# Optimization experiments

Measured on AMD Instinct MI355X. Metric: run time of the kernel, lower is better.

## Reference

```python
import jax, jax.numpy as jnp
import numpy as np

N_NODES = 20000
N_EDGES = 160000
N_GRAPHS = 1000
IN_DIM = 11
HID = 128
EDGE_DIM = 3
N_LAYERS = 5
BN_EPS = 1e-5


def setup_inputs() -> dict:
    key = jax.random.key(0)
    ks = jax.random.split(key, 24)
    x = jax.random.normal(ks[0], (N_NODES, IN_DIM), dtype=jnp.float32)
    edge_index = jax.random.randint(ks[1], (2, N_EDGES), 0, N_NODES, dtype=jnp.int64)
    batch = jnp.sort(jax.random.randint(ks[2], (N_NODES,), 0, N_GRAPHS, dtype=jnp.int64))
    edge_attr = jax.random.uniform(ks[3], (N_EDGES, EDGE_DIM), dtype=jnp.float32)
    s_in = 1.0 / np.sqrt(IN_DIM)
    s_z = 1.0 / np.sqrt(2 * HID + EDGE_DIM)
    s_h = 1.0 / np.sqrt(HID)
    W_in = jax.random.uniform(ks[4], (IN_DIM, HID), minval=-s_in, maxval=s_in)
    b_in = jax.random.uniform(ks[5], (HID,), minval=-s_in, maxval=s_in)
    Wf = jax.random.uniform(ks[6], (N_LAYERS, 2 * HID + EDGE_DIM, HID), minval=-s_z, maxval=s_z)
    bf = jax.random.uniform(ks[7], (N_LAYERS, HID), minval=-s_z, maxval=s_z)
    Ws = jax.random.uniform(ks[8], (N_LAYERS, 2 * HID + EDGE_DIM, HID), minval=-s_z, maxval=s_z)
    bs = jax.random.uniform(ks[9], (N_LAYERS, HID), minval=-s_z, maxval=s_z)
    gamma = jnp.ones((N_LAYERS, HID), dtype=jnp.float32)
    beta = jnp.zeros((N_LAYERS, HID), dtype=jnp.float32)
    W1 = jax.random.uniform(ks[10], (HID, HID), minval=-s_h, maxval=s_h)
    b1 = jax.random.uniform(ks[11], (HID,), minval=-s_h, maxval=s_h)
    W2 = jax.random.uniform(ks[12], (HID, HID), minval=-s_h, maxval=s_h)
    b2 = jax.random.uniform(ks[13], (HID,), minval=-s_h, maxval=s_h)
    W3 = jax.random.uniform(ks[14], (HID, 1), minval=-s_h, maxval=s_h)
    b3 = jax.random.uniform(ks[15], (1,), minval=-s_h, maxval=s_h)
    return {"x": x, "edge_index": edge_index, "batch": batch, "edge_attr": edge_attr,
            "W_in": W_in, "b_in": b_in, "Wf": Wf, "bf": bf, "Ws": Ws, "bs": bs,
            "gamma": gamma, "beta": beta, "W1": W1, "b1": b1, "W2": W2, "b2": b2,
            "W3": W3, "b3": b3}


def reference(x, edge_index, batch, edge_attr, W_in, b_in, Wf, bf, Ws, bs,
              gamma, beta, W1, b1, W2, b2, W3, b3):
    src = edge_index[0]  # x_j (source / neighbor)
    dst = edge_index[1]  # x_i (target / aggregation index)
    # in-degree per node for mean aggregation (zero-degree -> divide by 1, yields 0)
    deg = jax.ops.segment_sum(jnp.ones((N_EDGES,), jnp.float32), dst, num_segments=N_NODES)
    deg = jnp.maximum(deg, 1.0)[:, None]

    h = x @ W_in + b_in  # [N, H]
    for l in range(N_LAYERS):
        # CGConv: z = [x_i, x_j, e]; msg = sigmoid(z Wf) * softplus(z Ws); residual + mean-aggr
        z = jnp.concatenate([h[dst], h[src], edge_attr], axis=-1)  # [E, 2H+D]
        msg = jax.nn.sigmoid(z @ Wf[l] + bf[l]) * jax.nn.softplus(z @ Ws[l] + bs[l])
        agg = jax.ops.segment_sum(msg, dst, num_segments=N_NODES) / deg
        h = h + agg
        # BatchNorm1d (training-mode batch stats, biased variance)
        mu = jnp.mean(h, axis=0)
        var = jnp.mean((h - mu) ** 2, axis=0)
        h = (h - mu) * jax.lax.rsqrt(var + BN_EPS) * gamma[l] + beta[l]
        h = jax.nn.relu(h)
        # dropout omitted (eval mode)

    # global mean pool over graphs
    cnt = jax.ops.segment_sum(jnp.ones((N_NODES,), jnp.float32), batch, num_segments=N_GRAPHS)
    g = jax.ops.segment_sum(h, batch, num_segments=N_GRAPHS) / jnp.maximum(cnt, 1.0)[:, None]

    g = jax.nn.relu(g @ W1 + b1)
    g = jax.nn.relu(g @ W2 + b2)
    return g @ W3 + b3  # [G, 1]
```

## Files before the change

### kernel.cpp

```cpp
#include <hip/hip_runtime.h>
#include <hip/hip_cooperative_groups.h>
#include <math.h>

namespace cg = cooperative_groups;

#define NN 20000
#define NE 160000
#define NG 1000
#define IND 11
#define H 128
#define ED 3
#define NL 5
#define ZDH (259*128)
#define BN_EPSF 1e-5f
#define EPW 32
#define QR 16
#define GP 4
#define MBLK 313
#define NWIN (NE / EPW)
#define MEGA_BLOCKS 1024

#define DEG_BLKS ((NE + 255) / 256)
#define WPREP_BLKS ((NL * 512 * H + 255) / 256)
#define GB_BLKS ((NN + 255) / 256)
#define HIN_BLKS 512
#define PREP_GRID (DEG_BLKS + WPREP_BLKS + GB_BLKS + HIN_BLKS)

typedef unsigned short ushort_t;
typedef unsigned int uint_t;
typedef __attribute__((ext_vector_type(8))) short bf8_t;
typedef __attribute__((ext_vector_type(4))) float f4_t;

__device__ inline ushort_t f2bf(float x) {
    unsigned int u = __float_as_uint(x);
    unsigned int r = (u + 0x7fffu + ((u >> 16) & 1u)) >> 16;
    return (ushort_t)r;
}
__device__ inline float bf2f(ushort_t b) {
    return __uint_as_float(((unsigned int)b) << 16);
}

__global__ __launch_bounds__(256) void prep_fused(const int* __restrict__ dst,
                                                  int* __restrict__ degi,
                                                  const float* __restrict__ Wf,
                                                  const float* __restrict__ Ws,
                                                  ushort_t* __restrict__ Wt,
                                                  const float* __restrict__ x,
                                                  const float* __restrict__ Win,
                                                  const float* __restrict__ bin,
                                                  float* __restrict__ h,
                                                  const int* __restrict__ batch,
                                                  int* __restrict__ gstart) {
    int b = blockIdx.x;
    int tid = threadIdx.x;
    if (b < DEG_BLKS) {
        int e = b * 256 + tid;
        if (e < NE) atomicAdd(&degi[dst[e]], 1);
    } else if (b < DEG_BLKS + WPREP_BLKS) {
        int idx = (b - DEG_BLKS) * 256 + tid;
        if (idx < NL * 512 * H) {
            int k = idx & 127;
            int n = (idx >> 7) & 511;
            int l = idx >> 16;
            int t = n >> 7, j = n & 127;
            const float* W = (t == 0 || t == 2) ? Wf : Ws;
            int krow = (t < 2) ? k : (H + k);
            ushort_t val = f2bf(W[(size_t)l * ZDH + krow * H + j]);
            int nt = j >> 4, sub = j & 15;
            int ks = k >> 5, quad = (k >> 3) & 3, e2 = k & 7;
            int lane = quad * 16 + sub;
            Wt[(size_t)l * 65536 + (size_t)t * 16384 +
               (((nt * 4 + ks) * 64 + lane) * 8 + e2)] = val;
        }
    } else if (b < DEG_BLKS + WPREP_BLKS + GB_BLKS) {
        int n = (b - DEG_BLKS - WPREP_BLKS) * 256 + tid;
        if (n < NN) {
            int b0 = batch[n];
            int bn = (n + 1 < NN) ? batch[n + 1] : NG;
            if (n == 0)
                for (int t = 0; t <= b0; ++t) gstart[t] = 0;
            for (int t = b0 + 1; t <= bn; ++t) gstart[t] = n + 1;
        }
    } else {
        __shared__ float lw[IND * H];
        for (int i = tid; i < IND * H; i += 256) lw[i] = Win[i];
        __syncthreads();
        int j = tid & 127;
        float bj = bin[j];
        int rb = b - (DEG_BLKS + WPREP_BLKS + GB_BLKS);
        for (int n = rb * 2 + (tid >> 7); n < NN; n += HIN_BLKS * 2) {
            const float* xr = x + (size_t)n * IND;
            float acc = bj;
#pragma unroll
            for (int k = 0; k < IND; ++k) acc = fmaf(xr[k], lw[k * H + j], acc);
            h[(size_t)n * H + j] = acc;
        }
    }
}

__global__ __launch_bounds__(256) void reserve_kernel(const int* __restrict__ degi,
                                                      int* __restrict__ cursor,
                                                      float* __restrict__ invdeg,
                                                      int* __restrict__ counter,
                                                      unsigned* __restrict__ endmask) {
    int n = blockIdx.x * blockDim.x + threadIdx.x;
    int lane = threadIdx.x & 63;
    int v = (n < NN) ? degi[n] : 0;
    int x = v;
#pragma unroll
    for (int st = 1; st < 64; st <<= 1) {
        int y = __shfl_up(x, st, 64);
        if (lane >= st) x += y;
    }
    int total = __shfl(x, 63, 64);
    int base = 0;
    if (lane == 63) base = atomicAdd(counter, total);
    base = __shfl(base, 63, 64);
    if (n < NN) {
        int st0 = base + x - v;
        cursor[n] = st0;
        invdeg[n] = 1.0f / (float)(v < 1 ? 1 : v);
        if (v > 0) {
            int endp = st0 + v - 1;
            atomicOr(&endmask[endp >> 5], 1u << (endp & 31));
        }
    }
}

__global__ void scatter_kernel(const int* __restrict__ src, const int* __restrict__ dst,
                               const float* __restrict__ ea,
                               const float* __restrict__ invdeg,
                               int* __restrict__ cursor, float4* __restrict__ csr_ea4,
                               int* __restrict__ csr_dst, float* __restrict__ csr_inv) {
    int e = blockIdx.x * blockDim.x + threadIdx.x;
    if (e < NE) {
        int d = dst[e];
        int pos = atomicAdd(&cursor[d], 1);
        float4 r;
        r.x = ea[e * ED + 0];
        r.y = ea[e * ED + 1];
        r.z = ea[e * ED + 2];
        r.w = __int_as_float(src[e]);
        csr_ea4[pos] = r;
        csr_dst[pos] = d;
        csr_inv[pos] = invdeg[d];
    }
}


__device__ __forceinline__ void gemm_item(int mb, int pair,
                                          const float* __restrict__ hsrc,
                                          float* __restrict__ hbn,
                                          const ushort_t* __restrict__ Wt_l,
                                          const float* bnsc, const float* bnsh,
                                          int applyBN,
                                          uint_t* __restrict__ ppack,
                                          uint_t* __restrict__ qpack, int tid) {
    int wave = tid >> 6;
    int lane = tid & 63;
    int sub = lane & 15;
    int quad = lane >> 4;
    int m0 = mb * 64 + wave * 16;
    int writeH = applyBN && (pair == 0);

    const bf8_t* fragF = (const bf8_t*)(Wt_l + (size_t)(2 * pair) * 16384);
    const bf8_t* fragS = (const bf8_t*)(Wt_l + (size_t)(2 * pair + 1) * 16384);

    bf8_t aHi[4], aLo[4];
    int r = m0 + sub;
    int rc = r < NN ? r : NN - 1;
#pragma unroll
    for (int ks = 0; ks < 4; ++ks) {
        int kb = ks * 32 + quad * 8;
        const float* hp = hsrc + (size_t)rc * H + kb;
        float4 v0 = *(const float4*)hp;
        float4 v1 = *(const float4*)(hp + 4);
        float vv[8] = {v0.x, v0.y, v0.z, v0.w, v1.x, v1.y, v1.z, v1.w};
        if (applyBN) {
#pragma unroll
            for (int i = 0; i < 8; ++i) {
                float v = fmaf(vv[i], bnsc[kb + i], bnsh[kb + i]);
                vv[i] = v > 0.0f ? v : 0.0f;
            }
        }
        bf8_t hi8, lo8;
#pragma unroll
        for (int i = 0; i < 8; ++i) {
            ushort_t hi = f2bf(vv[i]);
            hi8[i] = (short)hi;
            lo8[i] = (short)f2bf(vv[i] - bf2f(hi));
        }
        aHi[ks] = hi8;
        aLo[ks] = lo8;
        if (writeH && r < NN) {
            float* op = hbn + (size_t)r * H + kb;
            *(float4*)op = make_float4(vv[0], vv[1], vv[2], vv[3]);
            *(float4*)(op + 4) = make_float4(vv[4], vv[5], vv[6], vv[7]);
        }
    }

    f4_t accF[8], accS[8];
#pragma unroll
    for (int b = 0; b < 8; ++b) { accF[b] = (f4_t){0.f, 0.f, 0.f, 0.f}; accS[b] = (f4_t){0.f, 0.f, 0.f, 0.f}; }

#pragma unroll
    for (int nt = 0; nt < 8; ++nt) {
#pragma unroll
        for (int ks = 0; ks < 4; ++ks) {
            bf8_t bF = fragF[(nt * 4 + ks) * 64 + lane];
            bf8_t bS = fragS[(nt * 4 + ks) * 64 + lane];
            accF[nt] = __builtin_amdgcn_mfma_f32_16x16x32_bf16(aHi[ks], bF, accF[nt], 0, 0, 0);
            accF[nt] = __builtin_amdgcn_mfma_f32_16x16x32_bf16(aLo[ks], bF, accF[nt], 0, 0, 0);
            accS[nt] = __builtin_amdgcn_mfma_f32_16x16x32_bf16(aHi[ks], bS, accS[nt], 0, 0, 0);
            accS[nt] = __builtin_amdgcn_mfma_f32_16x16x32_bf16(aLo[ks], bS, accS[nt], 0, 0, 0);
        }
    }

    uint_t* outp = pair ? qpack : ppack;
#pragma unroll
    for (int nt = 0; nt < 8; ++nt) {
        int col = nt * 16 + sub;
#pragma unroll
        for (int rr = 0; rr < 4; ++rr) {
            int row = m0 + quad * 4 + rr;
            if (row < NN) {
                uint_t lo = f2bf(accF[nt][rr]);
                uint_t hi = f2bf(accS[nt][rr]);
                outp[(size_t)row * H + col] = lo | (hi << 16);
            }
        }
    }
}

struct AggW { float2 wf0, wf1, wf2, ws0, ws1, ws2, bfv, bsv; };

__device__ __forceinline__ AggW load_aggw(const float* __restrict__ Wf_l,
                                          const float* __restrict__ bf_l,
                                          const float* __restrict__ Ws_l,
                                          const float* __restrict__ bs_l, int c0) {
    AggW a;
    a.wf0 = *(const float2*)&Wf_l[256 * H + c0];
    a.wf1 = *(const float2*)&Wf_l[257 * H + c0];
    a.wf2 = *(const float2*)&Wf_l[258 * H + c0];
    a.ws0 = *(const float2*)&Ws_l[256 * H + c0];
    a.ws1 = *(const float2*)&Ws_l[257 * H + c0];
    a.ws2 = *(const float2*)&Ws_l[258 * H + c0];
    a.bfv = *(const float2*)&bf_l[c0];
    a.bsv = *(const float2*)&bs_l[c0];
    return a;
}

__device__ __forceinline__ void agg_window(int base,
                                           const int4* __restrict__ csr_fe,
                                           const int* __restrict__ csr_dst,
                                           const float* __restrict__ csr_inv,
                                           const unsigned* __restrict__ endmask,
                                           const AggW& aw,
                                           const uint_t* __restrict__ ppack,
                                           const uint_t* __restrict__ qpack,
                                           float* __restrict__ h, int lane) {
    int c0 = 2 * lane;
    int4 fe = csr_fe[base + (lane & (EPW - 1))];
    int  dd = csr_dst[base + (lane & (EPW - 1))];
    int  ivr = __float_as_int(csr_inv[base + (lane & (EPW - 1))]);
    unsigned mask = __builtin_amdgcn_readfirstlane(endmask[base >> 5]);

    uint2 q[QR];
#pragma unroll
    for (int i = 0; i < QR; ++i) {
        int s = __builtin_amdgcn_readlane(fe.w, i);
        q[i] = *(const uint2*)&qpack[(size_t)s * H + c0];
    }

    int dcur = __builtin_amdgcn_readlane(dd, 0);
    uint2 ppc = *(const uint2*)&ppack[(size_t)dcur * H + c0];
    float pf0 = __uint_as_float(ppc.x << 16) + aw.bfv.x;
    float ps0 = __uint_as_float(ppc.x & 0xFFFF0000u) + aw.bsv.x;
    float pf1 = __uint_as_float(ppc.y << 16) + aw.bfv.y;
    float ps1 = __uint_as_float(ppc.y & 0xFFFF0000u) + aw.bsv.y;
    unsigned m = mask;
    int e0 = m ? __builtin_ctz(m) : EPW;
    int dnext = 0;
    uint2 ppN = ppc;
    if (e0 + 1 < EPW) {
        dnext = __builtin_amdgcn_readlane(dd, e0 + 1);
        ppN = *(const uint2*)&ppack[(size_t)dnext * H + c0];
    }

    float acc0 = 0.f, acc1 = 0.f;

#pragma unroll
    for (int tb = 0; tb < EPW; tb += 8) {
#pragma unroll
        for (int i = 0; i < 8; ++i) {
            int t = tb + i;
            float ex = __int_as_float(__builtin_amdgcn_readlane(fe.x, t));
            float ey = __int_as_float(__builtin_amdgcn_readlane(fe.y, t));
            float ez = __int_as_float(__builtin_amdgcn_readlane(fe.z, t));
            uint2 qq = q[t & (QR - 1)];
            if (t + QR < EPW) {
                int s2 = __builtin_amdgcn_readlane(fe.w, t + QR);
                q[t & (QR - 1)] = *(const uint2*)&qpack[(size_t)s2 * H + c0];
            }
            float qf0 = __uint_as_float(qq.x << 16);
            float qs0 = __uint_as_float(qq.x & 0xFFFF0000u);
            float qf1 = __uint_as_float(qq.y << 16);
            float qs1 = __uint_as_float(qq.y & 0xFFFF0000u);
            float f0 = fmaf(ex, aw.wf0.x, fmaf(ey, aw.wf1.x, fmaf(ez, aw.wf2.x, pf0 + qf0)));
            float v0 = fmaf(ex, aw.ws0.x, fmaf(ey, aw.ws1.x, fmaf(ez, aw.ws2.x, ps0 + qs0)));
            float f1 = fmaf(ex, aw.wf0.y, fmaf(ey, aw.wf1.y, fmaf(ez, aw.wf2.y, pf1 + qf1)));
            float v1 = fmaf(ex, aw.ws0.y, fmaf(ey, aw.ws1.y, fmaf(ez, aw.ws2.y, ps1 + qs1)));
            float sig0 = __builtin_amdgcn_rcpf(1.0f + __expf(-f0));
            float sp0  = fmaxf(v0, 0.0f) + __logf(1.0f + __expf(-fabsf(v0)));
            float sig1 = __builtin_amdgcn_rcpf(1.0f + __expf(-f1));
            float sp1  = fmaxf(v1, 0.0f) + __logf(1.0f + __expf(-fabsf(v1)));
            acc0 = fmaf(sig0, sp0, acc0);
            acc1 = fmaf(sig1, sp1, acc1);
            if (mask & (1u << t)) {
                float inv = __int_as_float(__builtin_amdgcn_readlane(ivr, t));
                atomicAdd(&h[(size_t)dcur * H + c0], acc0 * inv);
                atomicAdd(&h[(size_t)dcur * H + c0 + 1], acc1 * inv);
                acc0 = 0.f; acc1 = 0.f;
                dcur = dnext;
                pf0 = __uint_as_float(ppN.x << 16) + aw.bfv.x;
                ps0 = __uint_as_float(ppN.x & 0xFFFF0000u) + aw.bsv.x;
                pf1 = __uint_as_float(ppN.y << 16) + aw.bfv.y;
                ps1 = __uint_as_float(ppN.y & 0xFFFF0000u) + aw.bsv.y;
                m &= m - 1;
                int e1 = m ? __builtin_ctz(m) : EPW;
                if (e1 + 1 < EPW) {
                    dnext = __builtin_amdgcn_readlane(dd, e1 + 1);
                    ppN = *(const uint2*)&ppack[(size_t)dnext * H + c0];
                }
            }
        }
    }
    if (!(mask & (1u << (EPW - 1)))) {
        float inv = __int_as_float(__builtin_amdgcn_readlane(ivr, EPW - 1));
        atomicAdd(&h[(size_t)dcur * H + c0], acc0 * inv);
        atomicAdd(&h[(size_t)dcur * H + c0 + 1], acc1 * inv);
    }
}

__device__ __forceinline__ void stats_part(const float* __restrict__ h,
                                           float* __restrict__ sum,
                                           float* __restrict__ sumsq,
                                           int j, int part, int nparts) {
    float s = 0.0f, ss = 0.0f;
    for (int n = part * 8; n + 7 < NN; n += nparts * 8) {
        float v[8];
#pragma unroll
        for (int i = 0; i < 8; ++i) v[i] = h[(size_t)(n + i) * H + j];
#pragma unroll
        for (int i = 0; i < 8; ++i) { s += v[i]; ss = fmaf(v[i], v[i], ss); }
    }
    atomicAdd(&sum[j], s);
    atomicAdd(&sumsq[j], ss);
}

__global__ __launch_bounds__(256, 4) void mega_kernel(const int4* __restrict__ csr_fe,
                                                      const int* __restrict__ csr_dst,
                                                      const float* __restrict__ csr_inv,
                                                      const unsigned* __restrict__ endmask,
                                                      const float* __restrict__ Wf,
                                                      const float* __restrict__ bf,
                                                      const float* __restrict__ Ws,
                                                      const float* __restrict__ bs,
                                                      const ushort_t* __restrict__ Wt,
                                                      float* __restrict__ hA,
                                                      float* __restrict__ hB,
                                                      uint_t* __restrict__ ppack,
                                                      uint_t* __restrict__ qpack,
                                                      float* __restrict__ sum,
                                                      float* __restrict__ sumsq,
                                                      const float* __restrict__ gamma,
                                                      const float* __restrict__ beta) {
    cg::grid_group grid = cg::this_grid();
    __shared__ float bnsc[H];
    __shared__ float bnsh[H];
    int tid = threadIdx.x;
    int lane = tid & 63;
    int wv = tid >> 6;

    for (int l = 0; l < NL; ++l) {
        const float* hsrc = (l == 0) ? hA : ((l & 1) ? hA : hB);
        float* hTgt = (l == 0) ? hA : ((l & 1) ? hB : hA);
        const ushort_t* Wt_l = Wt + (size_t)l * 512 * H;
        int applyBN = (l > 0);

        if (applyBN) {
            if (tid < H) {
                float mu  = sum[tid] * (1.0f / NN);
                float var = sumsq[tid] * (1.0f / NN) - mu * mu;
                float sc  = gamma[(size_t)(l - 1) * H + tid] * rsqrtf(var + BN_EPSF);
                bnsc[tid] = sc;
                bnsh[tid] = beta[(size_t)(l - 1) * H + tid] - mu * sc;
            }
            __syncthreads();
        }
        for (int item = blockIdx.x; item < 2 * MBLK; item += gridDim.x) {
            int pair = item >= MBLK;
            gemm_item(pair ? item - MBLK : item, pair, hsrc, hTgt, Wt_l,
                      bnsc, bnsh, applyBN, ppack, qpack, tid);
        }
        grid.sync();

        if (blockIdx.x == 0 && tid < H) { sum[tid] = 0.0f; sumsq[tid] = 0.0f; }
        {
            AggW aw = load_aggw(Wf + (size_t)l * ZDH, bf + (size_t)l * H,
                                Ws + (size_t)l * ZDH, bs + (size_t)l * H, 2 * lane);
            for (int w = blockIdx.x * 4 + wv; w < NWIN; w += gridDim.x * 4)
                agg_window(w * EPW, csr_fe, csr_dst, csr_inv, endmask, aw,
                           ppack, qpack, hTgt, lane);
        }
        grid.sync();

        if (blockIdx.x < 256)
            stats_part(hTgt, sum, sumsq, tid & 127, blockIdx.x * 2 + (tid >> 7), 512);
        if (l < NL - 1) grid.sync();
    }
}

__global__ __launch_bounds__(256, 4) void node_gemm_mfma(const float* __restrict__ hsrc,
                                                         float* __restrict__ hbn,
                                                         const ushort_t* __restrict__ Wt_l,
                                                         const float* __restrict__ sum,
                                                         const float* __restrict__ sumsq,
                                                         const float* __restrict__ gamma_l,
                                                         const float* __restrict__ beta_l,
                                                         int applyBN,
                                                         uint_t* __restrict__ ppack,
                                                         uint_t* __restrict__ qpack) {
    __shared__ float bnsc[H];
    __shared__ float bnsh[H];
    int tid = threadIdx.x;
    if (applyBN) {
        if (tid < H) {
            float mu  = sum[tid] * (1.0f / NN);
            float var = sumsq[tid] * (1.0f / NN) - mu * mu;
            float sc  = gamma_l[tid] * rsqrtf(var + BN_EPSF);
            bnsc[tid] = sc;
            bnsh[tid] = beta_l[tid] - mu * sc;
        }
        __syncthreads();
    }
    gemm_item(blockIdx.x, blockIdx.y, hsrc, hbn, Wt_l, bnsc, bnsh,
              applyBN, ppack, qpack, tid);
}

__global__ __launch_bounds__(256) void agg_edge_kernel(const int4* __restrict__ csr_fe,
                                                       const int* __restrict__ csr_dst,
                                                       const float* __restrict__ csr_inv,
                                                       const unsigned* __restrict__ endmask,
                                                       const float* __restrict__ Wf_l,
                                                       const float* __restrict__ bf_l,
                                                       const float* __restrict__ Ws_l,
                                                       const float* __restrict__ bs_l,
                                                       const uint_t* __restrict__ ppack,
                                                       const uint_t* __restrict__ qpack,
                                                       float* __restrict__ h,
                                                       float* __restrict__ sum,
                                                       float* __restrict__ sumsq) {
    int tid = threadIdx.x;
    if (blockIdx.x == 0 && tid < H) { sum[tid] = 0.0f; sumsq[tid] = 0.0f; }
    int lane = tid & 63;
    int wv = tid >> 6;
    AggW aw = load_aggw(Wf_l, bf_l, Ws_l, bs_l, 2 * lane);
    agg_window((blockIdx.x * 4 + wv) * EPW, csr_fe, csr_dst, csr_inv, endmask, aw,
               ppack, qpack, h, lane);
}

__global__ __launch_bounds__(H) void stats_kernel(const float* __restrict__ h,
                                                  float* __restrict__ sum,
                                                  float* __restrict__ sumsq) {
    stats_part(h, sum, sumsq, threadIdx.x, blockIdx.x, gridDim.x);
}

__global__ __launch_bounds__(H) void pool_mlp_kernel(const float* __restrict__ h,
                                                     const int* __restrict__ gstart,
                                                     const float* __restrict__ sum,
                                                     const float* __restrict__ sumsq,
                                                     const float* __restrict__ gamma,
                                                     const float* __restrict__ beta,
                                                     const float* __restrict__ W1,
                                                     const float* __restrict__ b1,
                                                     const float* __restrict__ W2,
                                                     const float* __restrict__ b2,
                                                     const float* __restrict__ W3,
                                                     const float* __restrict__ b3,
                                                     float* __restrict__ out) {
    int j = threadIdx.x;
    float mu  = sum[j] * (1.0f / NN);
    float var = sumsq[j] * (1.0f / NN) - mu * mu;
    float sc  = gamma[j] * rsqrtf(var + BN_EPSF);
    float sh  = beta[j] - mu * sc;

    __shared__ float s1[GP][H];
    __shared__ float s2[GP][H];

#pragma unroll
    for (int gi = 0; gi < GP; ++gi) {
        int g0 = blockIdx.x * GP + gi;
        int a = gstart[g0], e = gstart[g0 + 1];
        float p0 = 0.f, p1 = 0.f, p2 = 0.f, p3 = 0.f;
        int n = a;
        for (; n + 3 < e; n += 4) {
            float v0 = fmaf(h[(size_t)(n + 0) * H + j], sc, sh);
            float v1 = fmaf(h[(size_t)(n + 1) * H + j], sc, sh);
            float v2 = fmaf(h[(size_t)(n + 2) * H + j], sc, sh);
            float v3 = fmaf(h[(size_t)(n + 3) * H + j], sc, sh);
            p0 += fmaxf(v0, 0.f); p1 += fmaxf(v1, 0.f);
            p2 += fmaxf(v2, 0.f); p3 += fmaxf(v3, 0.f);
        }
        for (; n < e; ++n) {
            float v = fmaf(h[(size_t)n * H + j], sc, sh);
            p0 += fmaxf(v, 0.f);
        }
        float cf = (float)(e - a);
        if (cf < 1.f) cf = 1.f;
        s1[gi][j] = ((p0 + p1) + (p2 + p3)) / cf;
    }
    __syncthreads();

    float a1[GP];
#pragma unroll
    for (int gi = 0; gi < GP; ++gi) a1[gi] = b1[j];
    for (int k = 0; k < H; ++k) {
        float w = W1[k * H + j];
#pragma unroll
        for (int gi = 0; gi < GP; ++gi) a1[gi] = fmaf(s1[gi][k], w, a1[gi]);
    }
#pragma unroll
    for (int gi = 0; gi < GP; ++gi) s2[gi][j] = fmaxf(a1[gi], 0.f);
    __syncthreads();

#pragma unroll
    for (int gi = 0; gi < GP; ++gi) a1[gi] = b2[j];
    for (int k = 0; k < H; ++k) {
        float w = W2[k * H + j];
#pragma unroll
        for (int gi = 0; gi < GP; ++gi) a1[gi] = fmaf(s2[gi][k], w, a1[gi]);
    }

    float w3 = W3[j];
    __shared__ float wred[2][GP];
#pragma unroll
    for (int gi = 0; gi < GP; ++gi) {
        float p = fmaxf(a1[gi], 0.f) * w3;
        for (int off2 = 32; off2 > 0; off2 >>= 1) p += __shfl_down(p, off2, 64);
        if ((j & 63) == 0) wred[j >> 6][gi] = p;
    }
    __syncthreads();
    if (j < GP) out[blockIdx.x * GP + j] = wred[0][j] + wred[1][j] + b3[0];
}

extern "C" void kernel_launch(void* const* d_in, const int* in_sizes, int n_in,
                              void* d_out, int out_size, void* d_ws, size_t ws_size,
                              hipStream_t stream) {
    const float* x     = (const float*)d_in[0];
    const int*   ei    = (const int*)d_in[1];
    const int*   srcp  = ei;
    const int*   dstp  = ei + NE;
    const int*   batch = (const int*)d_in[2];
    const float* ea    = (const float*)d_in[3];
    const float* Win   = (const float*)d_in[4];
    const float* bin   = (const float*)d_in[5];
    const float* Wf    = (const float*)d_in[6];
    const float* bf    = (const float*)d_in[7];
    const float* Ws    = (const float*)d_in[8];
    const float* bs    = (const float*)d_in[9];
    const float* gamma = (const float*)d_in[10];
    const float* beta  = (const float*)d_in[11];
    const float* W1    = (const float*)d_in[12];
    const float* b1    = (const float*)d_in[13];
    const float* W2    = (const float*)d_in[14];
    const float* b2    = (const float*)d_in[15];
    const float* W3    = (const float*)d_in[16];
    const float* b3    = (const float*)d_in[17];
    float* out = (float*)d_out;

    const size_t NH = (size_t)NN * H;
    float* wsp = (float*)d_ws;
    size_t off = 0;
    float* hA     = wsp + off; off += NH;
    float* hB     = wsp + off; off += NH;
    uint_t* ppack = (uint_t*)(wsp + off); off += NH;
    uint_t* qpack = (uint_t*)(wsp + off); off += NH;
    float* invdeg = wsp + off; off += NN;
    float* sum    = wsp + off; off += H;
    float* sumsq  = wsp + off; off += H;
    int* gstart   = (int*)(wsp + off); off += NG + 1;
    off = (off + 3) & ~(size_t)3;
    float4* csr_ea4 = (float4*)(wsp + off); off += (size_t)NE * 4;
    float* csr_inv = wsp + off; off += NE;
    int* degi      = (int*)(wsp + off); off += NN;
    int* counter   = (int*)(wsp + off); off += 1;
    unsigned* endmask = (unsigned*)(wsp + off); off += NE / 32;
    int* cursor    = (int*)(wsp + off); off += NN;
    int* csr_dst   = (int*)(wsp + off); off += NE;
    off = (off + 3) & ~(size_t)3;
    ushort_t* Wt = (ushort_t*)(wsp + off); off += (size_t)NL * 512 * H / 2;

    hipMemsetAsync(degi, 0, (NN + 1 + NE / 32) * sizeof(int), stream);
    prep_fused<<<PREP_GRID, 256, 0, stream>>>(dstp, degi, Wf, Ws, Wt,
                                              x, Win, bin, hA, batch, gstart);
    reserve_kernel<<<(NN + 255) / 256, 256, 0, stream>>>(degi, cursor, invdeg, counter,
                                                         endmask);
    scatter_kernel<<<(NE + 255) / 256, 256, 0, stream>>>(srcp, dstp, ea, invdeg, cursor,
                                                         csr_ea4, csr_dst, csr_inv);

    static int megaOK = -1;
    if (megaOK < 0) {
        int nb = 0;
        hipError_t oe = hipOccupancyMaxActiveBlocksPerMultiprocessor(&nb, mega_kernel, 256, 0);
        megaOK = (oe == hipSuccess && nb >= 4) ? 1 : 0;
    }
    bool megaDone = false;
    if (megaOK) {
        const int4* csr_fe_p = (const int4*)csr_ea4;
        const int* csr_dst_p = csr_dst;
        const float* csr_inv_p = csr_inv;
        const unsigned* endmask_p = endmask;
        const float* Wf_p = Wf;  const float* bf_p = bf;
        const float* Ws_p = Ws;  const float* bs_p = bs;
        const ushort_t* Wt_p = Wt;
        float* hA_p = hA;  float* hB_p = hB;
        uint_t* pp_p = ppack;  uint_t* qp_p = qpack;
        float* sum_p = sum;  float* sumsq_p = sumsq;
        const float* gamma_p = gamma;  const float* beta_p = beta;
        void* margs[] = {&csr_fe_p, &csr_dst_p, &csr_inv_p, &endmask_p,
                         &Wf_p, &bf_p, &Ws_p, &bs_p, &Wt_p,
                         &hA_p, &hB_p, &pp_p, &qp_p, &sum_p, &sumsq_p,
                         &gamma_p, &beta_p};
        hipError_t merr = hipLaunchCooperativeKernel(mega_kernel, dim3(MEGA_BLOCKS),
                                                     dim3(256), margs, 0, stream);
        if (merr == hipSuccess) megaDone = true;
        else (void)hipGetLastError();
    }
    float* hRead = hA;
    if (!megaDone) {
        hRead = hA;
        for (int l = 0; l < NL; ++l) {
            float* hTgt = (l == 0) ? hA : ((l & 1) ? hB : hA);
            node_gemm_mfma<<<dim3(MBLK, 2), 256, 0, stream>>>(
                hRead, hTgt, Wt + (size_t)l * 512 * H, sum, sumsq,
                gamma + (size_t)(l ? l - 1 : 0) * H,
                beta  + (size_t)(l ? l - 1 : 0) * H,
                l > 0, ppack, qpack);
            agg_edge_kernel<<<NWIN / 4, 256, 0, stream>>>((const int4*)csr_ea4, csr_dst,
                                                          csr_inv, endmask,
                                                          Wf + (size_t)l * ZDH, bf + (size_t)l * H,
                                                          Ws + (size_t)l * ZDH, bs + (size_t)l * H,
                                                          ppack, qpack, hTgt, sum, sumsq);
            stats_kernel<<<512, H, 0, stream>>>(hTgt, sum, sumsq);
            hRead = hTgt;
        }
    }

    pool_mlp_kernel<<<NG / GP, H, 0, stream>>>(hRead, gstart, sum, sumsq,
                                               gamma + (size_t)(NL - 1) * H,
                                               beta + (size_t)(NL - 1) * H,
                                               W1, b1, W2, b2, W3, b3, out);
}
```

Before: 453.6 us.

## Fold CSR preprocessing and pooling MLP into the cooperative mega kernel

Moves the memset, prep, reserve and scatter phases into the cooperative mega kernel as grid-strided work items separated by grid syncs. The final BN+ReLU, mean pooling and MLP head also run inside it on the first 250 blocks after a last grid sync. This is meant to remove five separate launches and their gaps. In exchange it adds extra grid-wide barriers, more shared memory per block that could lower occupancy, and long serial phases that run only a few blocks each.

```diff
diff --git a/kernel.cpp b/kernel.cpp
--- a/kernel.cpp
+++ b/kernel.cpp
@@ -24,7 +24,10 @@
 #define WPREP_BLKS ((NL * 512 * H + 255) / 256)
 #define GB_BLKS ((NN + 255) / 256)
 #define HIN_BLKS 512
-#define PREP_GRID (DEG_BLKS + WPREP_BLKS + GB_BLKS + HIN_BLKS)
+#define PREP_ITEMS (DEG_BLKS + WPREP_BLKS + GB_BLKS + HIN_BLKS)
+#define RSV_ITEMS ((NN + 255) / 256)
+#define SCAT_ITEMS ((NE + 255) / 256)
+#define ZERO_INTS (NN + 1 + NE / 32)
 
 typedef unsigned short ushort_t;
 typedef unsigned int uint_t;
@@ -40,19 +43,20 @@
     return __uint_as_float(((unsigned int)b) << 16);
 }
 
-__global__ __launch_bounds__(256) void prep_fused(const int* __restrict__ dst,
-                                                  int* __restrict__ degi,
-                                                  const float* __restrict__ Wf,
-                                                  const float* __restrict__ Ws,
-                                                  ushort_t* __restrict__ Wt,
-                                                  const float* __restrict__ x,
-                                                  const float* __restrict__ Win,
-                                                  const float* __restrict__ bin,
-                                                  float* __restrict__ h,
-                                                  const int* __restrict__ batch,
-                                                  int* __restrict__ gstart) {
-    int b = blockIdx.x;
-    int tid = threadIdx.x;
+
+__device__ __forceinline__ void prep_item(int b, int tid,
+                                          const int* __restrict__ dst,
+                                          int* __restrict__ degi,
+                                          const float* __restrict__ Wf,
+                                          const float* __restrict__ Ws,
+                                          ushort_t* __restrict__ Wt,
+                                          const float* __restrict__ x,
+                                          const float* __restrict__ Win,
+                                          const float* __restrict__ bin,
+                                          float* __restrict__ h,
+                                          const int* __restrict__ batch,
+                                          int* __restrict__ gstart,
+                                          float* lw ) {
     if (b < DEG_BLKS) {
         int e = b * 256 + tid;
         if (e < NE) atomicAdd(&degi[dst[e]], 1);
@@ -82,7 +86,6 @@
             for (int t = b0 + 1; t <= bn; ++t) gstart[t] = n + 1;
         }
     } else {
-        __shared__ float lw[IND * H];
         for (int i = tid; i < IND * H; i += 256) lw[i] = Win[i];
         __syncthreads();
         int j = tid & 127;
@@ -98,13 +101,14 @@
     }
 }
 
-__global__ __launch_bounds__(256) void reserve_kernel(const int* __restrict__ degi,
-                                                      int* __restrict__ cursor,
-                                                      float* __restrict__ invdeg,
-                                                      int* __restrict__ counter,
-                                                      unsigned* __restrict__ endmask) {
-    int n = blockIdx.x * blockDim.x + threadIdx.x;
-    int lane = threadIdx.x & 63;
+__device__ __forceinline__ void reserve_item(int b, int tid,
+                                             const int* __restrict__ degi,
+                                             int* __restrict__ cursor,
+                                             float* __restrict__ invdeg,
+                                             int* __restrict__ counter,
+                                             unsigned* __restrict__ endmask) {
+    int n = b * 256 + tid;
+    int lane = tid & 63;
     int v = (n < NN) ? degi[n] : 0;
     int x = v;
 #pragma unroll
@@ -127,12 +131,16 @@
     }
 }
 
-__global__ void scatter_kernel(const int* __restrict__ src, const int* __restrict__ dst,
-                               const float* __restrict__ ea,
-                               const float* __restrict__ invdeg,
-                               int* __restrict__ cursor, float4* __restrict__ csr_ea4,
-                               int* __restrict__ csr_dst, float* __restrict__ csr_inv) {
-    int e = blockIdx.x * blockDim.x + threadIdx.x;
+__device__ __forceinline__ void scatter_item(int b, int tid,
+                                             const int* __restrict__ src,
+                                             const int* __restrict__ dst,
+                                             const float* __restrict__ ea,
+                                             const float* __restrict__ invdeg,
+                                             int* __restrict__ cursor,
+                                             float4* __restrict__ csr_ea4,
+                                             int* __restrict__ csr_dst,
+                                             float* __restrict__ csr_inv) {
+    int e = b * 256 + tid;
     if (e < NE) {
         int d = dst[e];
         int pos = atomicAdd(&cursor[d], 1);
@@ -146,7 +154,6 @@
         csr_inv[pos] = invdeg[d];
     }
 }
-
 
 __device__ __forceinline__ void gemm_item(int mb, int pair,
                                           const float* __restrict__ hsrc,
@@ -358,29 +365,59 @@
     atomicAdd(&sumsq[j], ss);
 }
 
-__global__ __launch_bounds__(256, 4) void mega_kernel(const int4* __restrict__ csr_fe,
-                                                      const int* __restrict__ csr_dst,
-                                                      const float* __restrict__ csr_inv,
-                                                      const unsigned* __restrict__ endmask,
-                                                      const float* __restrict__ Wf,
-                                                      const float* __restrict__ bf,
-                                                      const float* __restrict__ Ws,
-                                                      const float* __restrict__ bs,
-                                                      const ushort_t* __restrict__ Wt,
-                                                      float* __restrict__ hA,
-                                                      float* __restrict__ hB,
-                                                      uint_t* __restrict__ ppack,
-                                                      uint_t* __restrict__ qpack,
-                                                      float* __restrict__ sum,
-                                                      float* __restrict__ sumsq,
-                                                      const float* __restrict__ gamma,
-                                                      const float* __restrict__ beta) {
+__global__ __launch_bounds__(256, 4) void mega_kernel(
+        const int* __restrict__ src, const int* __restrict__ dst,
+        const float* __restrict__ ea, const float* __restrict__ x,
+        const float* __restrict__ Win, const float* __restrict__ bin,
+        const int* __restrict__ batch,
+        int* __restrict__ degi, int* __restrict__ counter,
+        unsigned* __restrict__ endmask, int* __restrict__ cursor,
+        float* __restrict__ invdeg, float4* __restrict__ csr_ea4,
+        int* __restrict__ csr_dst, float* __restrict__ csr_inv,
+        int* __restrict__ gstart,
+        const float* __restrict__ Wf, const float* __restrict__ bf,
+        const float* __restrict__ Ws, const float* __restrict__ bs,
+        ushort_t* __restrict__ Wt,
+        float* __restrict__ hA, float* __restrict__ hB,
+        uint_t* __restrict__ ppack, uint_t* __restrict__ qpack,
+        float* __restrict__ sum, float* __restrict__ sumsq,
+        const float* __restrict__ gamma, const float* __restrict__ beta,
+        const float* __restrict__ W1, const float* __restrict__ b1,
+        const float* __restrict__ W2, const float* __restrict__ b2,
+        const float* __restrict__ W3, const float* __restrict__ b3,
+        float* __restrict__ out) {
     cg::grid_group grid = cg::this_grid();
     __shared__ float bnsc[H];
     __shared__ float bnsh[H];
+    __shared__ float lw[IND * H];
+    __shared__ float s1[GP][H];
+    __shared__ float s2[GP][H];
+    __shared__ float wred[2][GP];
     int tid = threadIdx.x;
     int lane = tid & 63;
     int wv = tid >> 6;
+
+    for (int i = blockIdx.x * 256 + tid; i < ZERO_INTS; i += gridDim.x * 256)
+        degi[i] = 0;
+    grid.sync();
+
+    for (int item = blockIdx.x; item < PREP_ITEMS; item += gridDim.x) {
+        prep_item(item, tid, dst, degi, Wf, Ws, Wt, x, Win, bin, hA, batch,
+                  gstart, lw);
+        __syncthreads();
+    }
+    grid.sync();
+
+    for (int item = blockIdx.x; item < RSV_ITEMS; item += gridDim.x)
+        reserve_item(item, tid, degi, cursor, invdeg, counter, endmask);
+    grid.sync();
+
+    for (int item = blockIdx.x; item < SCAT_ITEMS; item += gridDim.x)
+        scatter_item(item, tid, src, dst, ea, invdeg, cursor,
+                     csr_ea4, csr_dst, csr_inv);
+    grid.sync();
+
+    const int4* csr_fe = (const int4*)csr_ea4;
 
     for (int l = 0; l < NL; ++l) {
         const float* hsrc = (l == 0) ? hA : ((l & 1) ? hA : hB);
@@ -417,8 +454,110 @@
 
         if (blockIdx.x < 256)
             stats_part(hTgt, sum, sumsq, tid & 127, blockIdx.x * 2 + (tid >> 7), 512);
-        if (l < NL - 1) grid.sync();
-    }
+        grid.sync();
+    }
+
+    if (blockIdx.x < NG / GP) {
+        const float* h = hA;
+        const float* gam = gamma + (size_t)(NL - 1) * H;
+        const float* bet = beta + (size_t)(NL - 1) * H;
+        int j = tid;
+        if (j < H) {
+            float mu  = sum[j] * (1.0f / NN);
+            float var = sumsq[j] * (1.0f / NN) - mu * mu;
+            float sc  = gam[j] * rsqrtf(var + BN_EPSF);
+            float sh  = bet[j] - mu * sc;
+#pragma unroll
+            for (int gi = 0; gi < GP; ++gi) {
+                int g0 = blockIdx.x * GP + gi;
+                int a = gstart[g0], e = gstart[g0 + 1];
+                float p0 = 0.f, p1 = 0.f, p2 = 0.f, p3 = 0.f;
+                int n = a;
+                for (; n + 3 < e; n += 4) {
+                    float v0 = fmaf(h[(size_t)(n + 0) * H + j], sc, sh);
+                    float v1 = fmaf(h[(size_t)(n + 1) * H + j], sc, sh);
+                    float v2 = fmaf(h[(size_t)(n + 2) * H + j], sc, sh);
+                    float v3 = fmaf(h[(size_t)(n + 3) * H + j], sc, sh);
+                    p0 += fmaxf(v0, 0.f); p1 += fmaxf(v1, 0.f);
+                    p2 += fmaxf(v2, 0.f); p3 += fmaxf(v3, 0.f);
+                }
+                for (; n < e; ++n) {
+                    float v = fmaf(h[(size_t)n * H + j], sc, sh);
+                    p0 += fmaxf(v, 0.f);
+                }
+                float cf = (float)(e - a);
+                if (cf < 1.f) cf = 1.f;
+                s1[gi][j] = ((p0 + p1) + (p2 + p3)) / cf;
+            }
+        }
+        __syncthreads();
+
+        float a1[GP];
+        if (j < H) {
+#pragma unroll
+            for (int gi = 0; gi < GP; ++gi) a1[gi] = b1[j];
+            for (int k = 0; k < H; ++k) {
+                float w = W1[k * H + j];
+#pragma unroll
+                for (int gi = 0; gi < GP; ++gi) a1[gi] = fmaf(s1[gi][k], w, a1[gi]);
+            }
+#pragma unroll
+            for (int gi = 0; gi < GP; ++gi) s2[gi][j] = fmaxf(a1[gi], 0.f);
+        }
+        __syncthreads();
+
+        if (j < H) {
+#pragma unroll
+            for (int gi = 0; gi < GP; ++gi) a1[gi] = b2[j];
+            for (int k = 0; k < H; ++k) {
+                float w = W2[k * H + j];
+#pragma unroll
+                for (int gi = 0; gi < GP; ++gi) a1[gi] = fmaf(s2[gi][k], w, a1[gi]);
+            }
+            float w3 = W3[j];
+#pragma unroll
+            for (int gi = 0; gi < GP; ++gi) {
+                float p = fmaxf(a1[gi], 0.f) * w3;
+                for (int off2 = 32; off2 > 0; off2 >>= 1) p += __shfl_down(p, off2, 64);
+                if ((j & 63) == 0) wred[j >> 6][gi] = p;
+            }
+        }
+        __syncthreads();
+        if (tid < GP) out[blockIdx.x * GP + tid] = wred[0][tid] + wred[1][tid] + b3[0];
+    }
+}
+
+__global__ __launch_bounds__(256) void prep_fused(const int* __restrict__ dst,
+                                                  int* __restrict__ degi,
+                                                  const float* __restrict__ Wf,
+                                                  const float* __restrict__ Ws,
+                                                  ushort_t* __restrict__ Wt,
+                                                  const float* __restrict__ x,
+                                                  const float* __restrict__ Win,
+                                                  const float* __restrict__ bin,
+                                                  float* __restrict__ h,
+                                                  const int* __restrict__ batch,
+                                                  int* __restrict__ gstart) {
+    __shared__ float lw[IND * H];
+    prep_item(blockIdx.x, threadIdx.x, dst, degi, Wf, Ws, Wt, x, Win, bin, h,
+              batch, gstart, lw);
+}
+
+__global__ __launch_bounds__(256) void reserve_kernel(const int* __restrict__ degi,
+                                                      int* __restrict__ cursor,
+                                                      float* __restrict__ invdeg,
+                                                      int* __restrict__ counter,
+                                                      unsigned* __restrict__ endmask) {
+    reserve_item(blockIdx.x, threadIdx.x, degi, cursor, invdeg, counter, endmask);
+}
+
+__global__ void scatter_kernel(const int* __restrict__ src, const int* __restrict__ dst,
+                               const float* __restrict__ ea,
+                               const float* __restrict__ invdeg,
+                               int* __restrict__ cursor, float4* __restrict__ csr_ea4,
+                               int* __restrict__ csr_dst, float* __restrict__ csr_inv) {
+    scatter_item(blockIdx.x, threadIdx.x, src, dst, ea, invdeg, cursor,
+                 csr_ea4, csr_dst, csr_inv);
 }
 
 __global__ __launch_bounds__(256, 4) void node_gemm_mfma(const float* __restrict__ hsrc,
@@ -601,14 +740,6 @@
     off = (off + 3) & ~(size_t)3;
     ushort_t* Wt = (ushort_t*)(wsp + off); off += (size_t)NL * 512 * H / 2;
 
-    hipMemsetAsync(degi, 0, (NN + 1 + NE / 32) * sizeof(int), stream);
-    prep_fused<<<PREP_GRID, 256, 0, stream>>>(dstp, degi, Wf, Ws, Wt,
-                                              x, Win, bin, hA, batch, gstart);
-    reserve_kernel<<<(NN + 255) / 256, 256, 0, stream>>>(degi, cursor, invdeg, counter,
-                                                         endmask);
-    scatter_kernel<<<(NE + 255) / 256, 256, 0, stream>>>(srcp, dstp, ea, invdeg, cursor,
-                                                         csr_ea4, csr_dst, csr_inv);
-
     static int megaOK = -1;
     if (megaOK < 0) {
         int nb = 0;
@@ -617,29 +748,48 @@
     }
     bool megaDone = false;
     if (megaOK) {
-        const int4* csr_fe_p = (const int4*)csr_ea4;
-        const int* csr_dst_p = csr_dst;
-        const float* csr_inv_p = csr_inv;
-        const unsigned* endmask_p = endmask;
-        const float* Wf_p = Wf;  const float* bf_p = bf;
-        const float* Ws_p = Ws;  const float* bs_p = bs;
-        const ushort_t* Wt_p = Wt;
-        float* hA_p = hA;  float* hB_p = hB;
-        uint_t* pp_p = ppack;  uint_t* qp_p = qpack;
-        float* sum_p = sum;  float* sumsq_p = sumsq;
-        const float* gamma_p = gamma;  const float* beta_p = beta;
-        void* margs[] = {&csr_fe_p, &csr_dst_p, &csr_inv_p, &endmask_p,
+        const int* src_p = srcp; const int* dst_p = dstp;
+        const float* ea_p = ea; const float* x_p = x;
+        const float* Win_p = Win; const float* bin_p = bin;
+        const int* batch_p = batch;
+        int* degi_p = degi; int* counter_p = counter;
+        unsigned* endmask_p = endmask; int* cursor_p = cursor;
+        float* invdeg_p = invdeg; float4* csr_ea4_p = csr_ea4;
+        int* csr_dst_p = csr_dst; float* csr_inv_p = csr_inv;
+        int* gstart_p = gstart;
+        const float* Wf_p = Wf; const float* bf_p = bf;
+        const float* Ws_p = Ws; const float* bs_p = bs;
+        ushort_t* Wt_p = Wt;
+        float* hA_p = hA; float* hB_p = hB;
+        uint_t* pp_p = ppack; uint_t* qp_p = qpack;
+        float* sum_p = sum; float* sumsq_p = sumsq;
+        const float* gamma_p = gamma; const float* beta_p = beta;
+        const float* W1_p = W1; const float* b1_p = b1;
+        const float* W2_p = W2; const float* b2_p = b2;
+        const float* W3_p = W3; const float* b3_p = b3;
+        float* out_p = out;
+        void* margs[] = {&src_p, &dst_p, &ea_p, &x_p, &Win_p, &bin_p, &batch_p,
+                         &degi_p, &counter_p, &endmask_p, &cursor_p,
+                         &invdeg_p, &csr_ea4_p, &csr_dst_p, &csr_inv_p, &gstart_p,
                          &Wf_p, &bf_p, &Ws_p, &bs_p, &Wt_p,
                          &hA_p, &hB_p, &pp_p, &qp_p, &sum_p, &sumsq_p,
-                         &gamma_p, &beta_p};
+                         &gamma_p, &beta_p,
+                         &W1_p, &b1_p, &W2_p, &b2_p, &W3_p, &b3_p, &out_p};
         hipError_t merr = hipLaunchCooperativeKernel(mega_kernel, dim3(MEGA_BLOCKS),
                                                      dim3(256), margs, 0, stream);
         if (merr == hipSuccess) megaDone = true;
         else (void)hipGetLastError();
     }
-    float* hRead = hA;
+
     if (!megaDone) {
-        hRead = hA;
+        hipMemsetAsync(degi, 0, ZERO_INTS * sizeof(int), stream);
+        prep_fused<<<PREP_ITEMS, 256, 0, stream>>>(dstp, degi, Wf, Ws, Wt,
+                                                   x, Win, bin, hA, batch, gstart);
+        reserve_kernel<<<RSV_ITEMS, 256, 0, stream>>>(degi, cursor, invdeg, counter,
+                                                      endmask);
+        scatter_kernel<<<SCAT_ITEMS, 256, 0, stream>>>(srcp, dstp, ea, invdeg, cursor,
+                                                       csr_ea4, csr_dst, csr_inv);
+        float* hRead = hA;
         for (int l = 0; l < NL; ++l) {
             float* hTgt = (l == 0) ? hA : ((l & 1) ? hB : hA);
             node_gemm_mfma<<<dim3(MBLK, 2), 256, 0, stream>>>(
@@ -655,10 +805,9 @@
             stats_kernel<<<512, H, 0, stream>>>(hTgt, sum, sumsq);
             hRead = hTgt;
         }
-    }
-
-    pool_mlp_kernel<<<NG / GP, H, 0, stream>>>(hRead, gstart, sum, sumsq,
-                                               gamma + (size_t)(NL - 1) * H,
-                                               beta + (size_t)(NL - 1) * H,
-                                               W1, b1, W2, b2, W3, b3, out);
-}
+        pool_mlp_kernel<<<NG / GP, H, 0, stream>>>(hRead, gstart, sum, sumsq,
+                                                   gamma + (size_t)(NL - 1) * H,
+                                                   beta + (size_t)(NL - 1) * H,
+                                                   W1, b1, W2, b2, W3, b3, out);
+    }
+}
```

Measured after the change: 457.0 us. About the same (+0.7%).
